# Performance work log

Measured on AMD Instinct MI355X. Metric: run time of the kernel, lower is better.

Reference implementation:

```python
import jax, jax.numpy as jnp
import numpy as np

ALPHA = 0.2  # LeakyReLU negative slope


def setup_inputs() -> dict:
    key = jax.random.key(0)
    k1, k2, k3, k4, k5 = jax.random.split(key, 5)
    E, R, F = 256, 16, 64
    return {
        "h": jax.random.normal(k1, (E, F), dtype=jnp.float32),
        "r": jax.random.normal(k2, (R, F), dtype=jnp.float32),
        "adj": jax.random.normal(k3, (E, E, R), dtype=jnp.float32),
        "w_lin": jax.random.normal(k4, (1, F), dtype=jnp.float32) * (1.0 / np.sqrt(F)),
        "b_lin": jax.random.normal(k5, (1,), dtype=jnp.float32),
    }


def reference(h, r, adj, w_lin, b_lin):
    E, F = h.shape
    R = r.shape[0]
    # a_input[i,j,k,f] = h[i,f] * r[k,f] * h[j,f]   (torch repeat/view algebra)
    a_input = h[:, None, None, :] * h[None, :, None, :] * r[None, None, :, :]  # (E,E,R,F)
    adj_agg = jax.nn.softmax(adj, axis=1)  # (E,E,R)
    # leakyrelu over the big tensor, then reduce over the first E axis -> (E,R,F)
    attention = jnp.sum(jax.nn.leaky_relu(adj_agg[..., None] * a_input, ALPHA), axis=0)
    attention_E = jax.nn.softmax(attention, axis=0)  # softmax over E
    attention_R = jax.nn.softmax(attention, axis=1)  # softmax over R
    # linear (F -> 1) then torch .view(R, E, -1): a reshape, NOT a transpose
    alpha = (attention_R @ w_lin.T + b_lin).reshape(R, E, 1)
    alpha = jax.nn.softmax(alpha, axis=1)
    h_prime = jnp.sum(attention_E * h[:, None, :], axis=1)  # (E,F)
    r_prime = jnp.sum(attention_R * r[None, :, :], axis=0)  # (R,F)
    return jax.nn.elu(h_prime), jax.nn.elu(r_prime), alpha
```

## Files before the change

### kernel.cpp

```cpp
#include <hip/hip_runtime.h>
#include <math.h>


__device__ __forceinline__ float eluf(float x) { return x > 0.f ? x : expm1f(x); }

__global__ __launch_bounds__(256) void k1_softmax(const float* __restrict__ adj,
                                                  float* __restrict__ s) {
  __shared__ float red[64];
  const int b = blockIdx.x, t = threadIdx.x;
  const int lane = t & 63, wv = t >> 6;
  float v[16];
  const float4* a4 = (const float4*)(adj + b * 4096 + t * 16);
  float4 x0 = a4[0], x1 = a4[1], x2 = a4[2], x3 = a4[3];
  v[0]=x0.x; v[1]=x0.y; v[2]=x0.z; v[3]=x0.w;
  v[4]=x1.x; v[5]=x1.y; v[6]=x1.z; v[7]=x1.w;
  v[8]=x2.x; v[9]=x2.y; v[10]=x2.z; v[11]=x2.w;
  v[12]=x3.x; v[13]=x3.y; v[14]=x3.z; v[15]=x3.w;
  float m[16];
  #pragma unroll
  for (int k=0;k<16;++k) m[k]=v[k];
  #pragma unroll
  for (int off=1; off<64; off<<=1)
    #pragma unroll
    for (int k=0;k<16;++k) m[k] = fmaxf(m[k], __shfl_xor(m[k], off, 64));
  if (lane == 0) {
    #pragma unroll
    for (int k=0;k<16;++k) red[wv*16+k] = m[k];
  }
  __syncthreads();
  float sum[16];
  #pragma unroll
  for (int k=0;k<16;++k) {
    const float mk = fmaxf(fmaxf(red[k], red[16+k]), fmaxf(red[32+k], red[48+k]));
    v[k] = __expf(v[k] - mk);
    sum[k] = v[k];
  }
  #pragma unroll
  for (int off=1; off<64; off<<=1)
    #pragma unroll
    for (int k=0;k<16;++k) sum[k] += __shfl_xor(sum[k], off, 64);
  __syncthreads();
  if (lane == 0) {
    #pragma unroll
    for (int k=0;k<16;++k) red[wv*16+k] = sum[k];
  }
  __syncthreads();
  #pragma unroll
  for (int k=0;k<16;++k) {
    const float sk = red[k]+red[16+k]+red[32+k]+red[48+k];
    v[k] *= (1.f / sk);
  }
  float4* so4 = (float4*)(s + b*4096 + t*16);
  so4[0] = make_float4(v[0],v[1],v[2],v[3]);
  so4[1] = make_float4(v[4],v[5],v[6],v[7]);
  so4[2] = make_float4(v[8],v[9],v[10],v[11]);
  so4[3] = make_float4(v[12],v[13],v[14],v[15]);
}

__global__ __launch_bounds__(1024) void k2_contract(const float* __restrict__ h,
                                                    const float* __restrict__ r,
                                                    const float* __restrict__ s,
                                                    const float* __restrict__ w,
                                                    const float* __restrict__ bias,
                                                    float* __restrict__ att,
                                                    float* __restrict__ aR,
                                                    float* __restrict__ lin) {
  __shared__ float hl[256 * 64];
  __shared__ float redp[4 * 16 * 68];
  __shared__ float redq[4 * 16 * 68];
  __shared__ float attl[16 * 68];
  const int j = blockIdx.x, t = threadIdx.x;
  const int lane = t & 63, wv = t >> 6;

  float4* hl4 = (float4*)hl;
  const float4* h4 = (const float4*)h;
  #pragma unroll
  for (int q=0;q<4;++q) hl4[q*1024+t] = h4[q*1024+t];
  __syncthreads();

  const int kg = t >> 8, igH = (t >> 6) & 3, igL = (t >> 4) & 3, fg = t & 15;
  const int ig = igH*4 + igL;
  float p[4][4] = {};
  float qa[4][4] = {};
  const float* sjb = s + j*16 + kg*4;
  #pragma unroll 8
  for (int ii=0; ii<16; ++ii) {
    const int i = ig*16 + ii;
    const float4 sv = *(const float4*)(sjb + (size_t)i*4096);
    const float4 hv = *(const float4*)&hl[i*64 + fg*4];
    const float hvv[4] = {hv.x,hv.y,hv.z,hv.w};
    const float hav[4] = {fabsf(hv.x),fabsf(hv.y),fabsf(hv.z),fabsf(hv.w)};
    const float svv[4] = {sv.x,sv.y,sv.z,sv.w};
    #pragma unroll
    for (int kk=0;kk<4;++kk)
      #pragma unroll
      for (int ff=0;ff<4;++ff) {
        p[kk][ff]  = fmaf(svv[kk], hvv[ff], p[kk][ff]);
        qa[kk][ff] = fmaf(svv[kk], hav[ff], qa[kk][ff]);
      }
  }
  #pragma unroll
  for (int kk=0;kk<4;++kk)
    #pragma unroll
    for (int ff=0;ff<4;++ff) {
      p[kk][ff]  += __shfl_xor(p[kk][ff], 16, 64);
      p[kk][ff]  += __shfl_xor(p[kk][ff], 32, 64);
      qa[kk][ff] += __shfl_xor(qa[kk][ff], 16, 64);
      qa[kk][ff] += __shfl_xor(qa[kk][ff], 32, 64);
    }
  if (igL == 0) {
    #pragma unroll
    for (int kk=0;kk<4;++kk) {
      const int row = igH*16 + kg*4 + kk;
      *(float4*)&redp[row*68 + fg*4] = make_float4(p[kk][0],p[kk][1],p[kk][2],p[kk][3]);
      *(float4*)&redq[row*68 + fg*4] = make_float4(qa[kk][0],qa[kk][1],qa[kk][2],qa[kk][3]);
    }
  }
  __syncthreads();
  {
    const int k = t >> 6, f = t & 63;
    const int o = k*68 + f;
    const float pv = redp[o] + redp[1088+o] + redp[2176+o] + redp[3264+o];
    const float qv = redq[o] + redq[1088+o] + redq[2176+o] + redq[3264+o];
    const float c = hl[j*64+f] * r[k*64+f];
    const float av = 0.6f*c*pv + 0.4f*fabsf(c)*qv;
    attl[o] = av;
    att[j*1024 + t] = av;
  }
  __syncthreads();
  {
    const int f = lane;
    float mr = attl[f];
    #pragma unroll
    for (int k=1;k<16;++k) mr = fmaxf(mr, attl[k*68+f]);
    float ssum = 0.f;
    #pragma unroll
    for (int k=0;k<16;++k) ssum += __expf(attl[k*68+f]-mr);
    const float a = __expf(attl[wv*68+f]-mr) * (1.f/ssum);
    aR[j*1024 + wv*64 + f] = a;
    float vs = a * w[f];
    #pragma unroll
    for (int off=1; off<64; off<<=1) vs += __shfl_xor(vs, off, 64);
    if (f == 0) lin[j*16 + wv] = vs + bias[0];
  }
}

__global__ __launch_bounds__(256) void k3_colstats(const float* __restrict__ att,
                                                   const float* __restrict__ aR,
                                                   const float* __restrict__ r,
                                                   float* __restrict__ M,
                                                   float* __restrict__ Sinv,
                                                   float* __restrict__ out) {
  __shared__ float redm[4][16], reds[4][16], redr[4][16];
  const int b = blockIdx.x, t = threadIdx.x;
  const int lane = t & 63, wv = t >> 6;
  const int kfo = t & 15, eg = t >> 4;
  const int kf = b*16 + kfo;
  float av[16], rv[16];
  #pragma unroll
  for (int q=0;q<16;++q) {
    const int e = q*16 + eg;
    av[q] = att[e*1024 + kf];
    rv[q] = aR[e*1024 + kf];
  }
  float m = av[0];
  #pragma unroll
  for (int q=1;q<16;++q) m = fmaxf(m, av[q]);
  m = fmaxf(m, __shfl_xor(m, 16, 64));
  m = fmaxf(m, __shfl_xor(m, 32, 64));
  if (lane < 16) redm[wv][kfo] = m;
  __syncthreads();
  const float mc = fmaxf(fmaxf(redm[0][kfo], redm[1][kfo]),
                         fmaxf(redm[2][kfo], redm[3][kfo]));
  float es = 0.f, rs = 0.f;
  #pragma unroll
  for (int q=0;q<16;++q) { es += __expf(av[q]-mc); rs += rv[q]; }
  es += __shfl_xor(es, 16, 64); es += __shfl_xor(es, 32, 64);
  rs += __shfl_xor(rs, 16, 64); rs += __shfl_xor(rs, 32, 64);
  if (lane < 16) { reds[wv][kfo] = es; redr[wv][kfo] = rs; }
  __syncthreads();
  if (t < 16) {
    const int kf2 = b*16 + t;
    const float mt = fmaxf(fmaxf(redm[0][t], redm[1][t]),
                           fmaxf(redm[2][t], redm[3][t]));
    const float S  = reds[0][t] + reds[1][t] + reds[2][t] + reds[3][t];
    const float RS = redr[0][t] + redr[1][t] + redr[2][t] + redr[3][t];
    M[kf2] = mt;
    Sinv[kf2] = 1.f/S;
    out[16384 + kf2] = eluf(r[kf2] * RS);
  }
}

__global__ __launch_bounds__(64) void k4_final(const float* __restrict__ att,
                                               const float* __restrict__ lin,
                                               const float* __restrict__ h,
                                               const float* __restrict__ M,
                                               const float* __restrict__ Sinv,
                                               float* __restrict__ out) {
  const int b = blockIdx.x, t = threadIdx.x;
  if (b < 256) {
    const int e = b, f = t;
    float ssum = 0.f;
    #pragma unroll
    for (int k=0;k<16;++k) {
      const int kf = k*64 + f;
      ssum += __expf(att[e*1024 + kf] - M[kf]) * Sinv[kf];
    }
    out[e*64 + f] = eluf(h[e*64 + f] * ssum);
  } else {
    const int a = b - 256;
    float v[4];
    #pragma unroll
    for (int q=0;q<4;++q) v[q] = lin[a*256 + q*64 + t];
    float m2 = fmaxf(fmaxf(v[0],v[1]), fmaxf(v[2],v[3]));
    #pragma unroll
    for (int off=1; off<64; off<<=1) m2 = fmaxf(m2, __shfl_xor(m2, off, 64));
    float ex[4]; float ss = 0.f;
    #pragma unroll
    for (int q=0;q<4;++q) { ex[q] = __expf(v[q]-m2); ss += ex[q]; }
    #pragma unroll
    for (int off=1; off<64; off<<=1) ss += __shfl_xor(ss, off, 64);
    const float inv = 1.f/ss;
    #pragma unroll
    for (int q=0;q<4;++q) out[17408 + a*256 + q*64 + t] = ex[q]*inv;
  }
}

extern "C" void kernel_launch(void* const* d_in, const int* in_sizes, int n_in,
                              void* d_out, int out_size, void* d_ws, size_t ws_size,
                              hipStream_t stream) {
  (void)in_sizes; (void)n_in; (void)out_size; (void)ws_size;
  const float* h   = (const float*)d_in[0];
  const float* r   = (const float*)d_in[1];
  const float* adj = (const float*)d_in[2];
  const float* w   = (const float*)d_in[3];
  const float* bi  = (const float*)d_in[4];
  float* out = (float*)d_out;

  float* ws   = (float*)d_ws;
  float* s    = ws;
  float* att  = ws + 1048576;
  float* aR   = ws + 1310720;
  float* lin  = ws + 1572864;
  float* M    = ws + 1576960;
  float* Sinv = ws + 1577984;

  hipLaunchKernelGGL(k1_softmax,   dim3(256), dim3(256),  0, stream, adj, s);
  hipLaunchKernelGGL(k2_contract,  dim3(256), dim3(1024), 0, stream, h, r, s, w, bi, att, aR, lin);
  hipLaunchKernelGGL(k3_colstats,  dim3(64),  dim3(256),  0, stream, att, aR, r, M, Sinv, out);
  hipLaunchKernelGGL(k4_final,     dim3(272), dim3(64),   0, stream, att, lin, h, M, Sinv, out);
}
```

Measured before the change: 87.95 us.

## Recompute adjacency softmax in contraction kernel and merge final kernels

The first kernel now writes only per-column max and inverse sum instead of the full normalized softmax tensor. The contraction kernel recomputes each softmax weight from adj and these stats while staging a tile into shared memory. The aR intermediate is dropped because the row softmax is recomputed in a merged final kernel that handles the column stats, h_prime, r_prime and the alpha softmax. This removes a 4 MB write and read plus one launch. In exchange it adds extra exp work and shared memory in the contraction kernel, and the fused final kernel runs fewer, heavier blocks.

```diff
diff --git a/kernel.cpp b/kernel.cpp
--- a/kernel.cpp
+++ b/kernel.cpp
@@ -4,9 +4,10 @@
 
 __device__ __forceinline__ float eluf(float x) { return x > 0.f ? x : expm1f(x); }
 
-__global__ __launch_bounds__(256) void k1_softmax(const float* __restrict__ adj,
-                                                  float* __restrict__ s) {
+__global__ __launch_bounds__(256) void k1_stats(const float* __restrict__ adj,
+                                                float2* __restrict__ mS) {
   __shared__ float red[64];
+  __shared__ float mk[16];
   const int b = blockIdx.x, t = threadIdx.x;
   const int lane = t & 63, wv = t >> 6;
   float v[16];
@@ -28,13 +29,11 @@
     for (int k=0;k<16;++k) red[wv*16+k] = m[k];
   }
   __syncthreads();
+  if (t < 16) mk[t] = fmaxf(fmaxf(red[t], red[16+t]), fmaxf(red[32+t], red[48+t]));
+  __syncthreads();
   float sum[16];
   #pragma unroll
-  for (int k=0;k<16;++k) {
-    const float mk = fmaxf(fmaxf(red[k], red[16+k]), fmaxf(red[32+k], red[48+k]));
-    v[k] = __expf(v[k] - mk);
-    sum[k] = v[k];
-  }
+  for (int k=0;k<16;++k) sum[k] = __expf(v[k] - mk[k]);
   #pragma unroll
   for (int off=1; off<64; off<<=1)
     #pragma unroll
@@ -45,27 +44,22 @@
     for (int k=0;k<16;++k) red[wv*16+k] = sum[k];
   }
   __syncthreads();
-  #pragma unroll
-  for (int k=0;k<16;++k) {
-    const float sk = red[k]+red[16+k]+red[32+k]+red[48+k];
-    v[k] *= (1.f / sk);
-  }
-  float4* so4 = (float4*)(s + b*4096 + t*16);
-  so4[0] = make_float4(v[0],v[1],v[2],v[3]);
-  so4[1] = make_float4(v[4],v[5],v[6],v[7]);
-  so4[2] = make_float4(v[8],v[9],v[10],v[11]);
-  so4[3] = make_float4(v[12],v[13],v[14],v[15]);
+  if (t < 16) {
+    const float S = red[t] + red[16+t] + red[32+t] + red[48+t];
+    mS[b*16 + t] = make_float2(mk[t], 1.f / S);
+  }
 }
 
 __global__ __launch_bounds__(1024) void k2_contract(const float* __restrict__ h,
                                                     const float* __restrict__ r,
-                                                    const float* __restrict__ s,
+                                                    const float* __restrict__ adj,
+                                                    const float2* __restrict__ mS,
                                                     const float* __restrict__ w,
                                                     const float* __restrict__ bias,
                                                     float* __restrict__ att,
-                                                    float* __restrict__ aR,
                                                     float* __restrict__ lin) {
   __shared__ float hl[256 * 64];
+  __shared__ float sl[256 * 16];
   __shared__ float redp[4 * 16 * 68];
   __shared__ float redq[4 * 16 * 68];
   __shared__ float attl[16 * 68];
@@ -76,17 +70,29 @@
   const float4* h4 = (const float4*)h;
   #pragma unroll
   for (int q=0;q<4;++q) hl4[q*1024+t] = h4[q*1024+t];
+  {
+    const int v0 = t * 4;
+    const int i = v0 >> 4, k0 = v0 & 15;
+    const float4 av = *(const float4*)(adj + (size_t)i*4096 + j*16 + k0);
+    const float2 m0 = mS[i*16+k0+0], m1 = mS[i*16+k0+1];
+    const float2 m2 = mS[i*16+k0+2], m3 = mS[i*16+k0+3];
+    float4 sv;
+    sv.x = __expf(av.x - m0.x) * m0.y;
+    sv.y = __expf(av.y - m1.x) * m1.y;
+    sv.z = __expf(av.z - m2.x) * m2.y;
+    sv.w = __expf(av.w - m3.x) * m3.y;
+    *(float4*)&sl[i*16 + k0] = sv;
+  }
   __syncthreads();
 
   const int kg = t >> 8, igH = (t >> 6) & 3, igL = (t >> 4) & 3, fg = t & 15;
   const int ig = igH*4 + igL;
   float p[4][4] = {};
   float qa[4][4] = {};
-  const float* sjb = s + j*16 + kg*4;
   #pragma unroll 8
   for (int ii=0; ii<16; ++ii) {
     const int i = ig*16 + ii;
-    const float4 sv = *(const float4*)(sjb + (size_t)i*4096);
+    const float4 sv = *(const float4*)&sl[i*16 + kg*4];
     const float4 hv = *(const float4*)&hl[i*64 + fg*4];
     const float hvv[4] = {hv.x,hv.y,hv.z,hv.w};
     const float hav[4] = {fabsf(hv.x),fabsf(hv.y),fabsf(hv.z),fabsf(hv.w)};
@@ -137,7 +143,6 @@
     #pragma unroll
     for (int k=0;k<16;++k) ssum += __expf(attl[k*68+f]-mr);
     const float a = __expf(attl[wv*68+f]-mr) * (1.f/ssum);
-    aR[j*1024 + wv*64 + f] = a;
     float vs = a * w[f];
     #pragma unroll
     for (int off=1; off<64; off<<=1) vs += __shfl_xor(vs, off, 64);
@@ -145,84 +150,96 @@
   }
 }
 
-__global__ __launch_bounds__(256) void k3_colstats(const float* __restrict__ att,
-                                                   const float* __restrict__ aR,
-                                                   const float* __restrict__ r,
-                                                   float* __restrict__ M,
-                                                   float* __restrict__ Sinv,
-                                                   float* __restrict__ out) {
-  __shared__ float redm[4][16], reds[4][16], redr[4][16];
+__global__ __launch_bounds__(256) void k3_final(const float* __restrict__ att,
+                                               const float* __restrict__ lin,
+                                               const float* __restrict__ h,
+                                               const float* __restrict__ r,
+                                               float* __restrict__ out) {
+  __shared__ float red[4][17];
+  __shared__ float red16[3][4][16];
+  __shared__ float Mf[16], Sf[16];
   const int b = blockIdx.x, t = threadIdx.x;
   const int lane = t & 63, wv = t >> 6;
-  const int kfo = t & 15, eg = t >> 4;
-  const int kf = b*16 + kfo;
-  float av[16], rv[16];
-  #pragma unroll
-  for (int q=0;q<16;++q) {
-    const int e = q*16 + eg;
-    av[q] = att[e*1024 + kf];
-    rv[q] = aR[e*1024 + kf];
-  }
-  float m = av[0];
-  #pragma unroll
-  for (int q=1;q<16;++q) m = fmaxf(m, av[q]);
-  m = fmaxf(m, __shfl_xor(m, 16, 64));
-  m = fmaxf(m, __shfl_xor(m, 32, 64));
-  if (lane < 16) redm[wv][kfo] = m;
-  __syncthreads();
-  const float mc = fmaxf(fmaxf(redm[0][kfo], redm[1][kfo]),
-                         fmaxf(redm[2][kfo], redm[3][kfo]));
-  float es = 0.f, rs = 0.f;
-  #pragma unroll
-  for (int q=0;q<16;++q) { es += __expf(av[q]-mc); rs += rv[q]; }
-  es += __shfl_xor(es, 16, 64); es += __shfl_xor(es, 32, 64);
-  rs += __shfl_xor(rs, 16, 64); rs += __shfl_xor(rs, 32, 64);
-  if (lane < 16) { reds[wv][kfo] = es; redr[wv][kfo] = rs; }
-  __syncthreads();
-  if (t < 16) {
-    const int kf2 = b*16 + t;
-    const float mt = fmaxf(fmaxf(redm[0][t], redm[1][t]),
-                           fmaxf(redm[2][t], redm[3][t]));
-    const float S  = reds[0][t] + reds[1][t] + reds[2][t] + reds[3][t];
-    const float RS = redr[0][t] + redr[1][t] + redr[2][t] + redr[3][t];
-    M[kf2] = mt;
-    Sinv[kf2] = 1.f/S;
-    out[16384 + kf2] = eluf(r[kf2] * RS);
-  }
-}
-
-__global__ __launch_bounds__(64) void k4_final(const float* __restrict__ att,
-                                               const float* __restrict__ lin,
-                                               const float* __restrict__ h,
-                                               const float* __restrict__ M,
-                                               const float* __restrict__ Sinv,
-                                               float* __restrict__ out) {
-  const int b = blockIdx.x, t = threadIdx.x;
-  if (b < 256) {
-    const int e = b, f = t;
-    float ssum = 0.f;
-    #pragma unroll
-    for (int k=0;k<16;++k) {
-      const int kf = k*64 + f;
-      ssum += __expf(att[e*1024 + kf] - M[kf]) * Sinv[kf];
-    }
-    out[e*64 + f] = eluf(h[e*64 + f] * ssum);
+  if (b < 64) {
+    const int f = b, e = t;
+    float v[16];
+    #pragma unroll
+    for (int k=0;k<16;++k) v[k] = att[e*1024 + k*64 + f];
+    float cm[16];
+    #pragma unroll
+    for (int k=0;k<16;++k) cm[k] = v[k];
+    #pragma unroll
+    for (int off=1; off<64; off<<=1)
+      #pragma unroll
+      for (int k=0;k<16;++k) cm[k] = fmaxf(cm[k], __shfl_xor(cm[k], off, 64));
+    if (lane == 0) {
+      #pragma unroll
+      for (int k=0;k<16;++k) red16[0][wv][k] = cm[k];
+    }
+    float rm = v[0];
+    #pragma unroll
+    for (int k=1;k<16;++k) rm = fmaxf(rm, v[k]);
+    float ex[16]; float rs = 0.f;
+    #pragma unroll
+    for (int k=0;k<16;++k) { ex[k] = __expf(v[k]-rm); rs += ex[k]; }
+    const float rinv = 1.f/rs;
+    #pragma unroll
+    for (int k=0;k<16;++k) ex[k] *= rinv;
+    #pragma unroll
+    for (int off=1; off<64; off<<=1)
+      #pragma unroll
+      for (int k=0;k<16;++k) ex[k] += __shfl_xor(ex[k], off, 64);
+    if (lane == 0) {
+      #pragma unroll
+      for (int k=0;k<16;++k) red16[1][wv][k] = ex[k];
+    }
+    __syncthreads();
+    if (t < 16) {
+      Mf[t] = fmaxf(fmaxf(red16[0][0][t], red16[0][1][t]),
+                    fmaxf(red16[0][2][t], red16[0][3][t]));
+    }
+    __syncthreads();
+    float se[16];
+    #pragma unroll
+    for (int k=0;k<16;++k) se[k] = __expf(v[k] - Mf[k]);
+    #pragma unroll
+    for (int off=1; off<64; off<<=1)
+      #pragma unroll
+      for (int k=0;k<16;++k) se[k] += __shfl_xor(se[k], off, 64);
+    if (lane == 0) {
+      #pragma unroll
+      for (int k=0;k<16;++k) red16[2][wv][k] = se[k];
+    }
+    __syncthreads();
+    if (t < 16) {
+      const float S = red16[2][0][t] + red16[2][1][t] + red16[2][2][t] + red16[2][3][t];
+      Sf[t] = 1.f / S;
+      const float RS = red16[1][0][t] + red16[1][1][t] + red16[1][2][t] + red16[1][3][t];
+      out[16384 + t*64 + f] = eluf(r[t*64 + f] * RS);
+    }
+    __syncthreads();
+    float hp = 0.f;
+    #pragma unroll
+    for (int k=0;k<16;++k) hp += __expf(v[k] - Mf[k]) * Sf[k];
+    out[e*64 + f] = eluf(h[e*64 + f] * hp);
   } else {
-    const int a = b - 256;
-    float v[4];
-    #pragma unroll
-    for (int q=0;q<4;++q) v[q] = lin[a*256 + q*64 + t];
-    float m2 = fmaxf(fmaxf(v[0],v[1]), fmaxf(v[2],v[3]));
+    const int a = b - 64;
+    const float lv = lin[a*256 + t];
+    float m2 = lv;
     #pragma unroll
     for (int off=1; off<64; off<<=1) m2 = fmaxf(m2, __shfl_xor(m2, off, 64));
-    float ex[4]; float ss = 0.f;
-    #pragma unroll
-    for (int q=0;q<4;++q) { ex[q] = __expf(v[q]-m2); ss += ex[q]; }
+    if (lane == 0) red[wv][0] = m2;
+    __syncthreads();
+    m2 = fmaxf(fmaxf(red[0][0], red[1][0]), fmaxf(red[2][0], red[3][0]));
+    const float ex = __expf(lv - m2);
+    float ss = ex;
     #pragma unroll
     for (int off=1; off<64; off<<=1) ss += __shfl_xor(ss, off, 64);
-    const float inv = 1.f/ss;
-    #pragma unroll
-    for (int q=0;q<4;++q) out[17408 + a*256 + q*64 + t] = ex[q]*inv;
+    __syncthreads();
+    if (lane == 0) red[wv][1] = ss;
+    __syncthreads();
+    ss = red[0][1] + red[1][1] + red[2][1] + red[3][1];
+    out[17408 + a*256 + t] = ex * (1.f/ss);
   }
 }
 
@@ -238,15 +255,11 @@
   float* out = (float*)d_out;
 
   float* ws   = (float*)d_ws;
-  float* s    = ws;
-  float* att  = ws + 1048576;
-  float* aR   = ws + 1310720;
-  float* lin  = ws + 1572864;
-  float* M    = ws + 1576960;
-  float* Sinv = ws + 1577984;
-
-  hipLaunchKernelGGL(k1_softmax,   dim3(256), dim3(256),  0, stream, adj, s);
-  hipLaunchKernelGGL(k2_contract,  dim3(256), dim3(1024), 0, stream, h, r, s, w, bi, att, aR, lin);
-  hipLaunchKernelGGL(k3_colstats,  dim3(64),  dim3(256),  0, stream, att, aR, r, M, Sinv, out);
-  hipLaunchKernelGGL(k4_final,     dim3(272), dim3(64),   0, stream, att, lin, h, M, Sinv, out);
-}
+  float* att  = ws;
+  float* lin  = ws + 262144;
+  float2* mS  = (float2*)(ws + 266240);
+
+  hipLaunchKernelGGL(k1_stats,    dim3(256), dim3(256),  0, stream, adj, mS);
+  hipLaunchKernelGGL(k2_contract, dim3(256), dim3(1024), 0, stream, h, r, adj, mS, w, bi, att, lin);
+  hipLaunchKernelGGL(k3_final,    dim3(80),  dim3(256),  0, stream, att, lin, h, r, out);
+}
```

Result: no change. 88.55 us (+0.7%).
